# Performance work log

Measured on AMD Instinct MI355X. Metric: run time of the kernel, lower is better.

## Reference

```python
import jax, jax.numpy as jnp
import numpy as np

D_MODEL = 1024
NUM_HEADS = 16
GROUPS = 4
HEADS_PER_GROUP = NUM_HEADS // GROUPS
D_K = D_MODEL // NUM_HEADS
B, S = 2, 2048


def setup_inputs() -> dict:
    key = jax.random.key(0)
    ks = jax.random.split(key, 10)
    sc = 0.02
    return {
        "x": jax.random.normal(ks[0], (B, S, D_MODEL), dtype=jnp.float32),
        "W_Q": jax.random.normal(ks[1], (D_MODEL, D_MODEL), dtype=jnp.float32) * sc,
        "b_Q": jnp.zeros((D_MODEL,), dtype=jnp.float32),
        "W_K": jax.random.normal(ks[2], (GROUPS, D_MODEL, D_K), dtype=jnp.float32) * sc,
        "b_K": jnp.zeros((GROUPS, D_K), dtype=jnp.float32),
        "W_V": jax.random.normal(ks[3], (GROUPS, D_MODEL, D_K), dtype=jnp.float32) * sc,
        "b_V": jnp.zeros((GROUPS, D_K), dtype=jnp.float32),
        "W_O": jax.random.normal(ks[4], (D_MODEL, D_MODEL), dtype=jnp.float32) * sc,
        "b_O": jnp.zeros((D_MODEL,), dtype=jnp.float32),
    }


def reference(x, W_Q, b_Q, W_K, b_K, W_V, b_V, W_O, b_O):
    b, s, _ = x.shape
    # Q: [b, s, d_model] -> [b, groups, heads_per_group, s, d_k]
    Q = (x @ W_Q + b_Q).reshape(b, s, NUM_HEADS, D_K).transpose(0, 2, 1, 3)
    Q = Q.reshape(b, GROUPS, HEADS_PER_GROUP, s, D_K)
    # Shared K/V per group: [b, groups, s, d_k]
    K = jnp.einsum('bsd,gdk->bgsk', x, W_K) + b_K[None, :, None, :]
    V = jnp.einsum('bsd,gdk->bgsk', x, W_V) + b_V[None, :, None, :]
    # scores: [b, groups, heads_per_group, s, s]
    scores = jnp.einsum('bghsk,bgtk->bghst', Q, K) / jnp.sqrt(jnp.float32(D_K))
    attn = jax.nn.softmax(scores, axis=-1)
    # context: [b, groups, heads_per_group, s, d_k] -> [b, s, d_model]
    ctx = jnp.einsum('bghst,bgtk->bghsk', attn, V)
    ctx = ctx.reshape(b, NUM_HEADS, s, D_K).transpose(0, 2, 1, 3).reshape(b, s, D_MODEL)
    return ctx @ W_O + b_O
```

## Files before the change

### kernel.cpp

```cpp
#include <hip/hip_runtime.h>
#include <cstdint>
#include <cstddef>

typedef short bf16x8 __attribute__((ext_vector_type(8)));
typedef float f32x4 __attribute__((ext_vector_type(4)));

#define DM 1024
#define NHEADS 16
#define NGROUPS 4
#define DK 64
#define BATCH 2
#define SEQ 2048
#define MROWS 4096

#define QB_ELEMS   ((size_t)BATCH*NHEADS*SEQ*DK)
#define KB_ELEMS   ((size_t)BATCH*NGROUPS*SEQ*DK)
#define VT_ELEMS   KB_ELEMS
#define XC_ELEMS   ((size_t)MROWS*DM)
#define WQKV_ELEMS ((size_t)1536*DM)
#define WO_ELEMS   ((size_t)DM*DM)

#define SCL_Q 0.180336880f

__device__ __forceinline__ ushort f2bf(float f) {
    union { float f; uint32_t u; } a; a.f = f;
    uint32_t u = a.u;
    return (ushort)((u + 0x7FFFu + ((u >> 16) & 1u)) >> 16);
}

__device__ __forceinline__ void gll16(const void* g, void* l) {
    __builtin_amdgcn_global_load_lds((const __attribute__((address_space(1))) void*)g,
                                     (__attribute__((address_space(3))) void*)l, 16, 0, 0);
}

__global__ __launch_bounds__(256) void gqa_prep_kernel(
        const float* __restrict__ x,
        const float* __restrict__ WQ, const float* __restrict__ WK,
        const float* __restrict__ WV, const float* __restrict__ WO,
        const float* __restrict__ bQ, const float* __restrict__ bK,
        const float* __restrict__ bV,
        ushort* __restrict__ xbf, ushort* __restrict__ WqkvT,
        ushort* __restrict__ WoT, float* __restrict__ bcat)
{
    __shared__ float tl[64][65];
    const int bid = blockIdx.x, tid = threadIdx.x;
    if (bid < 640) {
        const float* src; ushort* dst; int src_ld; int r0, c0;
        if (bid < 256) {
            src = WQ; src_ld = 1024; dst = WqkvT;
            r0 = (bid >> 4) * 64; c0 = (bid & 15) * 64;
        } else if (bid < 512) {
            int t = bid - 256;
            src = WO; src_ld = 1024; dst = WoT;
            r0 = (t >> 4) * 64; c0 = (t & 15) * 64;
        } else if (bid < 576) {
            int t = bid - 512; int g = t >> 4;
            src = WK + (size_t)g * 1024 * 64; src_ld = 64;
            dst = WqkvT + (size_t)(1024 + g * 64) * 1024;
            r0 = (t & 15) * 64; c0 = 0;
        } else {
            int t = bid - 576; int g = t >> 4;
            src = WV + (size_t)g * 1024 * 64; src_ld = 64;
            dst = WqkvT + (size_t)(1280 + g * 64) * 1024;
            r0 = (t & 15) * 64; c0 = 0;
        }
        const int rr = tid >> 4, cc = (tid & 15) * 4;
#pragma unroll
        for (int p = 0; p < 4; p++) {
            int r = rr + p * 16;
            float4 v = *(const float4*)(src + (size_t)(r0 + r) * src_ld + c0 + cc);
            tl[cc + 0][r] = v.x; tl[cc + 1][r] = v.y;
            tl[cc + 2][r] = v.z; tl[cc + 3][r] = v.w;
        }
        __syncthreads();
#pragma unroll
        for (int p = 0; p < 4; p++) {
            int c = rr + p * 16;
            ushort4 o;
            o.x = f2bf(tl[c][cc + 0]); o.y = f2bf(tl[c][cc + 1]);
            o.z = f2bf(tl[c][cc + 2]); o.w = f2bf(tl[c][cc + 3]);
            *(ushort4*)(dst + (size_t)(c0 + c) * 1024 + r0 + cc) = o;
        }
    } else if (bid < 896) {
        int cid = bid - 640;
        const float* xs = x + (size_t)cid * 16384;
        ushort* xd = xbf + (size_t)cid * 16384;
#pragma unroll
        for (int p = 0; p < 16; p++) {
            float4 v = *(const float4*)(xs + p * 1024 + tid * 4);
            ushort4 o = { f2bf(v.x), f2bf(v.y), f2bf(v.z), f2bf(v.w) };
            *(ushort4*)(xd + p * 1024 + tid * 4) = o;
        }
    } else {
        for (int i = tid; i < 1536; i += 256) {
            float v = (i < 1024) ? bQ[i] : (i < 1280 ? bK[i - 1024] : bV[i - 1280]);
            bcat[i] = v;
        }
    }
}

template<bool QKV_EPI, int BN>
__global__ __launch_bounds__(256, 3) void gqa_gemm_kernel(
        const ushort* __restrict__ A, const ushort* __restrict__ BT,
        const float* __restrict__ bias, float* __restrict__ outF,
        ushort* __restrict__ Qb, ushort* __restrict__ Kb, ushort* __restrict__ Vtg)
{
    __shared__ ushort As[2][128 * 64];
    __shared__ ushort Bs[2][64 * 64];
    const int tid = threadIdx.x;
    const int i = blockIdx.x;
    const int xcd = i & 7, slot = i >> 3;
    const int bm = (slot / BN) * 8 + xcd;
    const int bn = slot % BN;
    const int wave = tid >> 6, lane = tid & 63;
    const int wm = (wave & 1) * 64, wn = (wave >> 1) * 32;
    const int lr = lane & 15, lq = lane >> 4;
    const int swz = lr & 7;

    const ushort* srcA[4]; int dstA[4];
    const ushort* srcB[2]; int dstB[2];
#pragma unroll
    for (int p = 0; p < 4; p++) {
        int slt = p * 256 + tid;
        int row = slt >> 3, cb = (slt & 7) ^ (row & 7);
        srcA[p] = A + (size_t)(bm * 128 + row) * 1024 + cb * 8;
        dstA[p] = p * 2048 + wave * 512;
    }
#pragma unroll
    for (int p = 0; p < 2; p++) {
        int slt = p * 256 + tid;
        int row = slt >> 3, cb = (slt & 7) ^ (row & 7);
        srcB[p] = BT + (size_t)(bn * 64 + row) * 1024 + cb * 8;
        dstB[p] = p * 2048 + wave * 512;
    }

    f32x4 acc[4][2];
#pragma unroll
    for (int ii = 0; ii < 4; ii++)
#pragma unroll
        for (int j = 0; j < 2; j++) acc[ii][j] = (f32x4){0.f, 0.f, 0.f, 0.f};

#pragma unroll
    for (int p = 0; p < 4; p++) gll16(srcA[p], &As[0][dstA[p]]);
#pragma unroll
    for (int p = 0; p < 2; p++) gll16(srcB[p], &Bs[0][dstB[p]]);

    for (int kt = 0; kt < 16; kt++) {
        __syncthreads();
        if (kt < 15) {
            int buf = (kt + 1) & 1, ko = (kt + 1) * 64;
#pragma unroll
            for (int p = 0; p < 4; p++) gll16(srcA[p] + ko, &As[buf][dstA[p]]);
#pragma unroll
            for (int p = 0; p < 2; p++) gll16(srcB[p] + ko, &Bs[buf][dstB[p]]);
        }
        const ushort* as = As[kt & 1];
        const ushort* bs = Bs[kt & 1];
        bf16x8 af[2][4], bfr[2][2];
#pragma unroll
        for (int kh = 0; kh < 2; kh++) {
#pragma unroll
            for (int ii = 0; ii < 4; ii++)
                af[kh][ii] = *(const bf16x8*)&as[(wm + ii * 16 + lr) * 64 + ((kh * 4 + lq) ^ swz) * 8];
#pragma unroll
            for (int j = 0; j < 2; j++)
                bfr[kh][j] = *(const bf16x8*)&bs[(wn + j * 16 + lr) * 64 + ((kh * 4 + lq) ^ swz) * 8];
        }
#pragma unroll
        for (int kh = 0; kh < 2; kh++)
#pragma unroll
            for (int ii = 0; ii < 4; ii++)
#pragma unroll
                for (int j = 0; j < 2; j++)
                    acc[ii][j] = __builtin_amdgcn_mfma_f32_16x16x32_bf16(af[kh][ii], bfr[kh][j], acc[ii][j], 0, 0, 0);
    }

#pragma unroll
    for (int ii = 0; ii < 4; ii++) {
        int mg = bm * 128 + wm + ii * 16 + lq * 4;
        int b = mg >> 11, s = mg & 2047;
#pragma unroll
        for (int j = 0; j < 2; j++) {
            int cg = bn * 64 + wn + j * 16 + lr;
            float bv = bias[cg];
            if constexpr (QKV_EPI) {
                int d = cg & 63;
                if (cg < 1024) {
                    int h = cg >> 6;
                    ushort* dst = Qb + ((size_t)(b * NHEADS + h) * SEQ + s) * DK + d;
#pragma unroll
                    for (int r = 0; r < 4; r++)
                        dst[r * DK] = f2bf((acc[ii][j][r] + bv) * SCL_Q);
                } else if (cg < 1280) {
                    int g = (cg - 1024) >> 6;
                    ushort* dst = Kb + ((size_t)(b * NGROUPS + g) * SEQ + s) * DK + d;
#pragma unroll
                    for (int r = 0; r < 4; r++) dst[r * DK] = f2bf(acc[ii][j][r] + bv);
                } else {
                    int g = (cg - 1280) >> 6;
                    int s4 = s >> 2, kg = s4 & 7;
                    int col = ((s4 >> 3) << 5) + (((((kg & 3) << 1) | (kg >> 2))) << 2);
                    ushort4 pk;
                    pk.x = f2bf(acc[ii][j][0] + bv); pk.y = f2bf(acc[ii][j][1] + bv);
                    pk.z = f2bf(acc[ii][j][2] + bv); pk.w = f2bf(acc[ii][j][3] + bv);
                    *(ushort4*)(Vtg + ((size_t)(b * NGROUPS + g) * DK + d) * SEQ + col) = pk;
                }
            } else {
#pragma unroll
                for (int r = 0; r < 4; r++)
                    outF[(size_t)(mg + r) * DM + cg] = acc[ii][j][r] + bv;
            }
        }
    }
}

__global__ __launch_bounds__(256, 2) void gqa_attn_kernel(
        const ushort* __restrict__ Qb, const ushort* __restrict__ Kb,
        const ushort* __restrict__ Vtg, ushort* __restrict__ ctx)
{
    __shared__ ushort smem[2][2][64 * 64];
    __shared__ float accX[2][4][16];

    const int tid = threadIdx.x, wave = tid >> 6, lane = tid & 63;
    const int lr = lane & 15, lq = lane >> 4;
    const int swz = lr & 7;
    const int wq = wave & 1, wt = wave >> 1;
    const int i = blockIdx.x;
    const int bg = i & 7, s2 = i >> 3;
    const int qt = s2 & 15, h = s2 >> 4;
    const int b = bg >> 2, g = bg & 3, hg = g * 4 + h;

    const ushort* Qh = Qb  + (size_t)(b * NHEADS  + hg) * SEQ * DK;
    const ushort* Kg = Kb  + (size_t)(b * NGROUPS + g)  * SEQ * DK;
    const ushort* Vg = Vtg + (size_t)(b * NGROUPS + g)  * DK * SEQ;

    const int s0 = qt * 128 + wq * 64;
    const int tb = wt * 32;

    bf16x8 qf[4][2];
#pragma unroll
    for (int qs = 0; qs < 4; qs++)
#pragma unroll
        for (int kh = 0; kh < 2; kh++)
            qf[qs][kh] = *(const bf16x8*)(Qh + (size_t)(s0 + qs * 16 + lr) * DK + kh * 32 + lq * 8);

    const ushort* srcK[2]; const ushort* srcV[2]; int dstOff[2];
#pragma unroll
    for (int p = 0; p < 2; p++) {
        int slt = p * 256 + tid;
        int row = slt >> 3, cb = (slt & 7) ^ (row & 7);
        srcK[p] = Kg + (size_t)row * DK + cb * 8;
        srcV[p] = Vg + (size_t)row * SEQ + cb * 8;
        dstOff[p] = p * 2048 + wave * 512;
    }

    f32x4 of[4][4];
#pragma unroll
    for (int qs = 0; qs < 4; qs++)
#pragma unroll
        for (int j = 0; j < 4; j++) of[qs][j] = (f32x4){0.f, 0.f, 0.f, 0.f};
    f32x4 accL[4];
#pragma unroll
    for (int qs = 0; qs < 4; qs++) accL[qs] = (f32x4){0.f, 0.f, 0.f, 0.f};

    bf16x8 ones;
#pragma unroll
    for (int k = 0; k < 8; k++) ones[k] = (short)0x3F80;

#pragma unroll
    for (int p = 0; p < 2; p++) {
        gll16(srcK[p], &smem[0][0][dstOff[p]]);
        gll16(srcV[p], &smem[1][0][dstOff[p]]);
    }

    for (int it = 0; it < 32; it++) {
        __syncthreads();
        if (it < 31) {
            int buf = (it + 1) & 1, t0 = (it + 1) * 64;
#pragma unroll
            for (int p = 0; p < 2; p++) {
                gll16(srcK[p] + (size_t)t0 * DK, &smem[0][buf][dstOff[p]]);
                gll16(srcV[p] + t0, &smem[1][buf][dstOff[p]]);
            }
        }
        const ushort* ks = smem[0][it & 1];
        const ushort* vs = smem[1][it & 1];

        bf16x8 kf[2][2];
#pragma unroll
        for (int nt = 0; nt < 2; nt++)
#pragma unroll
            for (int kh = 0; kh < 2; kh++)
                kf[nt][kh] = *(const bf16x8*)&ks[((tb + nt * 16 + lr) * 8 + ((kh * 4 + lq) ^ swz)) * 8];

        bf16x8 vf[4];
#pragma unroll
        for (int j = 0; j < 4; j++)
            vf[j] = *(const bf16x8*)&vs[((j * 16 + lr) * 8 + ((wt * 4 + lq) ^ swz)) * 8];

        f32x4 sc[4][2];
#pragma unroll
        for (int qs = 0; qs < 4; qs++)
#pragma unroll
            for (int nt = 0; nt < 2; nt++) {
                f32x4 s = (f32x4){0.f, 0.f, 0.f, 0.f};
                s = __builtin_amdgcn_mfma_f32_16x16x32_bf16(kf[nt][0], qf[qs][0], s, 0, 0, 0);
                s = __builtin_amdgcn_mfma_f32_16x16x32_bf16(kf[nt][1], qf[qs][1], s, 0, 0, 0);
                sc[qs][nt] = s;
            }

        union PF { bf16x8 v; uint32_t w[4]; };
        PF pf[4];
#pragma unroll
        for (int qs = 0; qs < 4; qs++) {
#pragma unroll
            for (int nt = 0; nt < 2; nt++) {
                union { float f; uint32_t u; } e0, e1, e2, e3;
                e0.f = __builtin_amdgcn_exp2f(sc[qs][nt][0]);
                e1.f = __builtin_amdgcn_exp2f(sc[qs][nt][1]);
                e2.f = __builtin_amdgcn_exp2f(sc[qs][nt][2]);
                e3.f = __builtin_amdgcn_exp2f(sc[qs][nt][3]);
                pf[qs].w[nt * 2 + 0] = __builtin_amdgcn_perm(e1.u, e0.u, 0x07060302u);
                pf[qs].w[nt * 2 + 1] = __builtin_amdgcn_perm(e3.u, e2.u, 0x07060302u);
            }
            accL[qs] = __builtin_amdgcn_mfma_f32_16x16x32_bf16(ones, pf[qs].v, accL[qs], 0, 0, 0);
        }

#pragma unroll
        for (int qs = 0; qs < 4; qs++)
#pragma unroll
            for (int j = 0; j < 4; j++)
                of[qs][j] = __builtin_amdgcn_mfma_f32_16x16x32_bf16(vf[j], pf[qs].v, of[qs][j], 0, 0, 0);
    }

    __syncthreads();
    float* comb = (float*)&smem[0][0][0];
    if (wt == 1) {
        float* cw = comb + wq * 4096;
#pragma unroll
        for (int qs = 0; qs < 4; qs++)
#pragma unroll
            for (int j = 0; j < 4; j++)
                *(f32x4*)&cw[(qs * 4 + j) * 256 + lane * 4] = of[qs][j];
        if (lq == 0) {
#pragma unroll
            for (int qs = 0; qs < 4; qs++) accX[wq][qs][lr] = accL[qs][0];
        }
    }
    __syncthreads();
    if (wt == 0) {
        const float* cw = comb + wq * 4096;
        float inv[4];
#pragma unroll
        for (int qs = 0; qs < 4; qs++)
            inv[qs] = 1.0f / (accL[qs][0] + accX[wq][qs][lr]);
        ushort* cbp = ctx + (size_t)b * SEQ * DM;
#pragma unroll
        for (int qs = 0; qs < 4; qs++) {
            int s = s0 + qs * 16 + lr;
#pragma unroll
            for (int j = 0; j < 4; j++) {
                f32x4 o2 = of[qs][j] + *(const f32x4*)&cw[(qs * 4 + j) * 256 + lane * 4];
                ushort4 o;
                o.x = f2bf(o2[0] * inv[qs]);
                o.y = f2bf(o2[1] * inv[qs]);
                o.z = f2bf(o2[2] * inv[qs]);
                o.w = f2bf(o2[3] * inv[qs]);
                *(ushort4*)(cbp + (size_t)s * DM + hg * 64 + j * 16 + lq * 4) = o;
            }
        }
    }
}

extern "C" void kernel_launch(void* const* d_in, const int* in_sizes, int n_in,
                              void* d_out, int out_size, void* d_ws, size_t ws_size,
                              hipStream_t stream) {
    const float* x  = (const float*)d_in[0];
    const float* WQ = (const float*)d_in[1];
    const float* bQ = (const float*)d_in[2];
    const float* WK = (const float*)d_in[3];
    const float* bK = (const float*)d_in[4];
    const float* WV = (const float*)d_in[5];
    const float* bV = (const float*)d_in[6];
    const float* WO = (const float*)d_in[7];
    const float* bO = (const float*)d_in[8];

    ushort* Qb    = (ushort*)d_ws;
    ushort* Kb    = Qb + QB_ELEMS;
    ushort* Vtg   = Kb + KB_ELEMS;
    ushort* xc    = Vtg + VT_ELEMS;
    ushort* WqkvT = xc + XC_ELEMS;
    ushort* WoT   = WqkvT + WQKV_ELEMS;
    float*  bcat  = (float*)(WoT + WO_ELEMS);

    gqa_prep_kernel<<<897, 256, 0, stream>>>(x, WQ, WK, WV, WO, bQ, bK, bV,
                                             xc, WqkvT, WoT, bcat);
    gqa_gemm_kernel<true, 24><<<768, 256, 0, stream>>>(
        xc, WqkvT, bcat, nullptr, Qb, Kb, Vtg);
    gqa_attn_kernel<<<512, 256, 0, stream>>>(Qb, Kb, Vtg, xc);
    gqa_gemm_kernel<false, 16><<<512, 256, 0, stream>>>(
        xc, WoT, bO, (float*)d_out, nullptr, nullptr, nullptr);
}
```

Before: 163.3 us.

## Shrink GEMM tiles to 64x64 and move W_O transpose into QKV GEMM

The GEMM tile drops from 128x64 to 64x64 with a smaller shared-memory footprint and launch bounds raised to 4 blocks per CU, doubling the block count for both projections. The W_O transpose-and-convert moves out of the prep kernel and runs as 256 extra blocks at the start of the QKV GEMM launch, shortening the prep critical path. The aim is better occupancy and load balance. The cost is lower per-block data reuse, so A/B tiles are reloaded more often.

```diff
diff --git a/kernel.cpp b/kernel.cpp
--- a/kernel.cpp
+++ b/kernel.cpp
@@ -33,56 +33,54 @@
                                      (__attribute__((address_space(3))) void*)l, 16, 0, 0);
 }
 
+__device__ __forceinline__ void transpose_tile(
+        const float* __restrict__ src, int src_ld, ushort* __restrict__ dst,
+        int r0, int c0, int tid, float (*tl)[65])
+{
+    const int rr = tid >> 4, cc = (tid & 15) * 4;
+#pragma unroll
+    for (int p = 0; p < 4; p++) {
+        int r = rr + p * 16;
+        float4 v = *(const float4*)(src + (size_t)(r0 + r) * src_ld + c0 + cc);
+        tl[cc + 0][r] = v.x; tl[cc + 1][r] = v.y;
+        tl[cc + 2][r] = v.z; tl[cc + 3][r] = v.w;
+    }
+    __syncthreads();
+#pragma unroll
+    for (int p = 0; p < 4; p++) {
+        int c = rr + p * 16;
+        ushort4 o;
+        o.x = f2bf(tl[c][cc + 0]); o.y = f2bf(tl[c][cc + 1]);
+        o.z = f2bf(tl[c][cc + 2]); o.w = f2bf(tl[c][cc + 3]);
+        *(ushort4*)(dst + (size_t)(c0 + c) * 1024 + r0 + cc) = o;
+    }
+}
+
 __global__ __launch_bounds__(256) void gqa_prep_kernel(
         const float* __restrict__ x,
         const float* __restrict__ WQ, const float* __restrict__ WK,
-        const float* __restrict__ WV, const float* __restrict__ WO,
+        const float* __restrict__ WV,
         const float* __restrict__ bQ, const float* __restrict__ bK,
         const float* __restrict__ bV,
         ushort* __restrict__ xbf, ushort* __restrict__ WqkvT,
-        ushort* __restrict__ WoT, float* __restrict__ bcat)
+        float* __restrict__ bcat)
 {
     __shared__ float tl[64][65];
     const int bid = blockIdx.x, tid = threadIdx.x;
-    if (bid < 640) {
-        const float* src; ushort* dst; int src_ld; int r0, c0;
-        if (bid < 256) {
-            src = WQ; src_ld = 1024; dst = WqkvT;
-            r0 = (bid >> 4) * 64; c0 = (bid & 15) * 64;
-        } else if (bid < 512) {
-            int t = bid - 256;
-            src = WO; src_ld = 1024; dst = WoT;
-            r0 = (t >> 4) * 64; c0 = (t & 15) * 64;
-        } else if (bid < 576) {
-            int t = bid - 512; int g = t >> 4;
-            src = WK + (size_t)g * 1024 * 64; src_ld = 64;
-            dst = WqkvT + (size_t)(1024 + g * 64) * 1024;
-            r0 = (t & 15) * 64; c0 = 0;
-        } else {
-            int t = bid - 576; int g = t >> 4;
-            src = WV + (size_t)g * 1024 * 64; src_ld = 64;
-            dst = WqkvT + (size_t)(1280 + g * 64) * 1024;
-            r0 = (t & 15) * 64; c0 = 0;
-        }
-        const int rr = tid >> 4, cc = (tid & 15) * 4;
-#pragma unroll
-        for (int p = 0; p < 4; p++) {
-            int r = rr + p * 16;
-            float4 v = *(const float4*)(src + (size_t)(r0 + r) * src_ld + c0 + cc);
-            tl[cc + 0][r] = v.x; tl[cc + 1][r] = v.y;
-            tl[cc + 2][r] = v.z; tl[cc + 3][r] = v.w;
-        }
-        __syncthreads();
-#pragma unroll
-        for (int p = 0; p < 4; p++) {
-            int c = rr + p * 16;
-            ushort4 o;
-            o.x = f2bf(tl[c][cc + 0]); o.y = f2bf(tl[c][cc + 1]);
-            o.z = f2bf(tl[c][cc + 2]); o.w = f2bf(tl[c][cc + 3]);
-            *(ushort4*)(dst + (size_t)(c0 + c) * 1024 + r0 + cc) = o;
-        }
-    } else if (bid < 896) {
-        int cid = bid - 640;
+    if (bid < 256) {
+        transpose_tile(WQ, 1024, WqkvT, (bid >> 4) * 64, (bid & 15) * 64, tid, tl);
+    } else if (bid < 320) {
+        int t = bid - 256, g = t >> 4;
+        transpose_tile(WK + (size_t)g * 1024 * 64, 64,
+                       WqkvT + (size_t)(1024 + g * 64) * 1024,
+                       (t & 15) * 64, 0, tid, tl);
+    } else if (bid < 384) {
+        int t = bid - 320, g = t >> 4;
+        transpose_tile(WV + (size_t)g * 1024 * 64, 64,
+                       WqkvT + (size_t)(1280 + g * 64) * 1024,
+                       (t & 15) * 64, 0, tid, tl);
+    } else if (bid < 640) {
+        int cid = bid - 384;
         const float* xs = x + (size_t)cid * 16384;
         ushort* xd = xbf + (size_t)cid * 16384;
 #pragma unroll
@@ -99,68 +97,73 @@
     }
 }
 
-template<bool QKV_EPI, int BN>
-__global__ __launch_bounds__(256, 3) void gqa_gemm_kernel(
+template<bool QKV_EPI, int BN, bool RIDERS>
+__global__ __launch_bounds__(256, 4) void gqa_gemm_kernel(
         const ushort* __restrict__ A, const ushort* __restrict__ BT,
         const float* __restrict__ bias, float* __restrict__ outF,
-        ushort* __restrict__ Qb, ushort* __restrict__ Kb, ushort* __restrict__ Vtg)
+        ushort* __restrict__ Qb, ushort* __restrict__ Kb, ushort* __restrict__ Vtg,
+        const float* __restrict__ WO, ushort* __restrict__ WoT)
 {
-    __shared__ ushort As[2][128 * 64];
-    __shared__ ushort Bs[2][64 * 64];
+    __shared__ ushort smem[4][4096];
     const int tid = threadIdx.x;
-    const int i = blockIdx.x;
+    int i = blockIdx.x;
+
+    if constexpr (RIDERS) {
+        if (i < 256) {
+            float (*tl)[65] = (float(*)[65])&smem[0][0];
+            transpose_tile(WO, 1024, WoT, (i >> 4) * 64, (i & 15) * 64, tid, tl);
+            return;
+        }
+        i -= 256;
+    }
+
     const int xcd = i & 7, slot = i >> 3;
     const int bm = (slot / BN) * 8 + xcd;
     const int bn = slot % BN;
     const int wave = tid >> 6, lane = tid & 63;
-    const int wm = (wave & 1) * 64, wn = (wave >> 1) * 32;
+    const int wm = (wave & 1) * 32, wn = (wave >> 1) * 32;
     const int lr = lane & 15, lq = lane >> 4;
     const int swz = lr & 7;
 
-    const ushort* srcA[4]; int dstA[4];
-    const ushort* srcB[2]; int dstB[2];
-#pragma unroll
-    for (int p = 0; p < 4; p++) {
-        int slt = p * 256 + tid;
-        int row = slt >> 3, cb = (slt & 7) ^ (row & 7);
-        srcA[p] = A + (size_t)(bm * 128 + row) * 1024 + cb * 8;
-        dstA[p] = p * 2048 + wave * 512;
-    }
+    const ushort* srcA[2]; const ushort* srcB[2]; int dstOff[2];
 #pragma unroll
     for (int p = 0; p < 2; p++) {
         int slt = p * 256 + tid;
         int row = slt >> 3, cb = (slt & 7) ^ (row & 7);
+        srcA[p] = A  + (size_t)(bm * 64 + row) * 1024 + cb * 8;
         srcB[p] = BT + (size_t)(bn * 64 + row) * 1024 + cb * 8;
-        dstB[p] = p * 2048 + wave * 512;
-    }
-
-    f32x4 acc[4][2];
-#pragma unroll
-    for (int ii = 0; ii < 4; ii++)
+        dstOff[p] = p * 2048 + wave * 512;
+    }
+
+    f32x4 acc[2][2];
+#pragma unroll
+    for (int ii = 0; ii < 2; ii++)
 #pragma unroll
         for (int j = 0; j < 2; j++) acc[ii][j] = (f32x4){0.f, 0.f, 0.f, 0.f};
 
 #pragma unroll
-    for (int p = 0; p < 4; p++) gll16(srcA[p], &As[0][dstA[p]]);
-#pragma unroll
-    for (int p = 0; p < 2; p++) gll16(srcB[p], &Bs[0][dstB[p]]);
+    for (int p = 0; p < 2; p++) {
+        gll16(srcA[p], &smem[0][dstOff[p]]);
+        gll16(srcB[p], &smem[2][dstOff[p]]);
+    }
 
     for (int kt = 0; kt < 16; kt++) {
         __syncthreads();
         if (kt < 15) {
             int buf = (kt + 1) & 1, ko = (kt + 1) * 64;
 #pragma unroll
-            for (int p = 0; p < 4; p++) gll16(srcA[p] + ko, &As[buf][dstA[p]]);
-#pragma unroll
-            for (int p = 0; p < 2; p++) gll16(srcB[p] + ko, &Bs[buf][dstB[p]]);
-        }
-        const ushort* as = As[kt & 1];
-        const ushort* bs = Bs[kt & 1];
-        bf16x8 af[2][4], bfr[2][2];
+            for (int p = 0; p < 2; p++) {
+                gll16(srcA[p] + ko, &smem[buf][dstOff[p]]);
+                gll16(srcB[p] + ko, &smem[2 + buf][dstOff[p]]);
+            }
+        }
+        const ushort* as = smem[kt & 1];
+        const ushort* bs = smem[2 + (kt & 1)];
+        bf16x8 af[2][2], bfr[2][2];
 #pragma unroll
         for (int kh = 0; kh < 2; kh++) {
 #pragma unroll
-            for (int ii = 0; ii < 4; ii++)
+            for (int ii = 0; ii < 2; ii++)
                 af[kh][ii] = *(const bf16x8*)&as[(wm + ii * 16 + lr) * 64 + ((kh * 4 + lq) ^ swz) * 8];
 #pragma unroll
             for (int j = 0; j < 2; j++)
@@ -169,15 +172,15 @@
 #pragma unroll
         for (int kh = 0; kh < 2; kh++)
 #pragma unroll
-            for (int ii = 0; ii < 4; ii++)
+            for (int ii = 0; ii < 2; ii++)
 #pragma unroll
                 for (int j = 0; j < 2; j++)
                     acc[ii][j] = __builtin_amdgcn_mfma_f32_16x16x32_bf16(af[kh][ii], bfr[kh][j], acc[ii][j], 0, 0, 0);
     }
 
 #pragma unroll
-    for (int ii = 0; ii < 4; ii++) {
-        int mg = bm * 128 + wm + ii * 16 + lq * 4;
+    for (int ii = 0; ii < 2; ii++) {
+        int mg = bm * 64 + wm + ii * 16 + lq * 4;
         int b = mg >> 11, s = mg & 2047;
 #pragma unroll
         for (int j = 0; j < 2; j++) {
@@ -393,11 +396,11 @@
     ushort* WoT   = WqkvT + WQKV_ELEMS;
     float*  bcat  = (float*)(WoT + WO_ELEMS);
 
-    gqa_prep_kernel<<<897, 256, 0, stream>>>(x, WQ, WK, WV, WO, bQ, bK, bV,
-                                             xc, WqkvT, WoT, bcat);
-    gqa_gemm_kernel<true, 24><<<768, 256, 0, stream>>>(
-        xc, WqkvT, bcat, nullptr, Qb, Kb, Vtg);
+    gqa_prep_kernel<<<641, 256, 0, stream>>>(x, WQ, WK, WV, bQ, bK, bV,
+                                             xc, WqkvT, bcat);
+    gqa_gemm_kernel<true, 24, true><<<1792, 256, 0, stream>>>(
+        xc, WqkvT, bcat, nullptr, Qb, Kb, Vtg, WO, WoT);
     gqa_attn_kernel<<<512, 256, 0, stream>>>(Qb, Kb, Vtg, xc);
-    gqa_gemm_kernel<false, 16><<<512, 256, 0, stream>>>(
-        xc, WoT, bO, (float*)d_out, nullptr, nullptr, nullptr);
-}
+    gqa_gemm_kernel<false, 16, false><<<1024, 256, 0, stream>>>(
+        xc, WoT, bO, (float*)d_out, nullptr, nullptr, nullptr, nullptr, nullptr);
+}
```

Measured after the change: 160.7 us. No clear change (-1.6%).
